# Optimization experiments

Hardware: AMD Instinct MI355X
Metric: run time of the kernel (lower is better)

## Reference

```python
import jax, jax.numpy as jnp
import numpy as np


def setup_inputs() -> dict:
    key = jax.random.key(0)
    k1, k2, k3 = jax.random.split(key, 3)
    B, V, J = 32, 100000, 52
    vertices = jax.random.normal(k1, (1, V, 3), dtype=jnp.float32)
    lbs_weights = jax.random.uniform(k2, (1, V, J), dtype=jnp.float32)
    skinning_transforms = jax.random.normal(k3, (B, J, 4, 4), dtype=jnp.float32)
    return {
        "vertices": vertices,
        "lbs_weights": lbs_weights,
        "skinning_transforms": skinning_transforms,
    }


def reference(vertices, lbs_weights, skinning_transforms):
    # 3D-vertices branch of Skinning.forward
    B = skinning_transforms.shape[0]
    J = skinning_transforms.shape[1]
    V = vertices.shape[1]
    # W: [B,V,J] (broadcast of [1,V,J]); T_flat: [B,V,16] -> T: [B,V,4,4]
    T = jnp.einsum(
        "bvj,bjx->bvx",
        jnp.broadcast_to(lbs_weights, (B, V, J)),
        skinning_transforms.reshape(B, J, 16),
    ).reshape(B, V, 4, 4)
    # homogeneous vertex coords [B,V,4]
    v_posed_homo = jnp.concatenate(
        [
            jnp.broadcast_to(vertices, (B, V, 3)),
            jnp.ones((B, V, 1), dtype=vertices.dtype),
        ],
        axis=2,
    )
    # per-vertex 4x4 @ 4 transform, keep xyz
    v_homo = jnp.einsum("bvij,bvj->bvi", T, v_posed_homo)
    return v_homo[:, :, :3]
```

## Files before the change

kernel.cpp:

```cpp
#include <hip/hip_runtime.h>
#include <hip/hip_bf16.h>


typedef __attribute__((ext_vector_type(8))) short bf16x8;
typedef __attribute__((ext_vector_type(4))) float f32x4;

constexpr int J      = 52;
constexpr int KSTEPS = 7;
constexpr int NT     = 6;
constexpr int WAVES  = 4;
constexpr int MT     = 2;
constexpr int VPW    = MT * 16;
constexpr int VPB    = WAVES * VPW;
constexpr int NSLOT  = KSTEPS * NT * 64;
constexpr int BP_B   = NSLOT * 16;
constexpr int SL_B   = 16 * VPW * 3 * 4;

__device__ __forceinline__ unsigned pk2(float a, float b) {
    __hip_bfloat162 h = __float22bfloat162_rn(make_float2(a, b));
    return *reinterpret_cast<unsigned*>(&h);
}

__global__ __launch_bounds__(256, 2) void skin_fused(
    const float* __restrict__ verts,
    const float* __restrict__ weights,
    const float* __restrict__ xf,
    float* __restrict__ out,
    int V)
{
    __shared__ __align__(16) char sBp[BP_B];
    __shared__ __align__(16) char sSl[WAVES][SL_B];

    const int tid  = threadIdx.x;
    const int lane = tid & 63;
    const int wid  = tid >> 6;
    const int lgrp = lane >> 4;
    const int lrow = lane & 15;
    const int v0   = blockIdx.x * VPB;
    const int v0w  = v0 + wid * VPW;

    float hx[MT], hy[MT], hz[MT];
    float2 wv[MT][KSTEPS];
#pragma unroll
    for (int mt = 0; mt < MT; ++mt) {
        const int v   = v0w + mt * 16 + lrow;
        const int vcl = (v < V) ? v : (V - 1);
        hx[mt] = verts[3 * (size_t)vcl + 0];
        hy[mt] = verts[3 * (size_t)vcl + 1];
        hz[mt] = verts[3 * (size_t)vcl + 2];
        const float* wr = weights + (size_t)vcl * J;
#pragma unroll
        for (int s = 0; s < KSTEPS; ++s) {
            const int j0 = s * 8 + lgrp * 2;
            wv[mt][s] = (j0 < J) ? *(const float2*)(wr + j0) : float2{0.f, 0.f};
        }
    }

    {
        const float4* __restrict__ xf4 = reinterpret_cast<const float4*>(xf);
        for (int slot = tid; slot < NSLOT; slot += 256) {
            const int s     = slot / (NT * 64);
            const int rem   = slot - s * (NT * 64);
            const int t     = rem >> 6;
            const int l     = rem & 63;
            const int plgrp = l >> 4;
            const int plrow = l & 15;
            const int n  = t * 16 + plrow;
            const int b  = n / 3;
            const int i  = n - 3 * b;
            const int j0 = s * 8 + plgrp * 2;
            float4 m0 = {0,0,0,0}, m1 = {0,0,0,0};
            if (j0 < J)     m0 = xf4[(b * J + j0) * 4 + i];
            if (j0 + 1 < J) m1 = xf4[(b * J + j0 + 1) * 4 + i];
            union { bf16x8 v; unsigned w[4]; } r;
            r.w[0] = pk2(m0.x, m0.y); r.w[1] = pk2(m0.z, m0.w);
            r.w[2] = pk2(m1.x, m1.y); r.w[3] = pk2(m1.z, m1.w);
            *(bf16x8*)(sBp + slot * 16) = r.v;
        }
    }
    __syncthreads();

    f32x4 acc[MT][NT];
#pragma unroll
    for (int mt = 0; mt < MT; ++mt)
#pragma unroll
        for (int t = 0; t < NT; ++t)
            acc[mt][t] = f32x4{0.f, 0.f, 0.f, 0.f};

#pragma unroll
    for (int s = 0; s < KSTEPS; ++s) {
        bf16x8 frag[NT];
#pragma unroll
        for (int t = 0; t < NT; ++t)
            frag[t] = *(const bf16x8*)(sBp + ((s * NT + t) * 64 + lane) * 16);
#pragma unroll
        for (int mt = 0; mt < MT; ++mt) {
            const float w0 = wv[mt][s].x, w1 = wv[mt][s].y;
            union { bf16x8 v; unsigned w[4]; } xf8;
            xf8.w[0] = pk2(w0 * hx[mt], w0 * hy[mt]);
            xf8.w[1] = pk2(w0 * hz[mt], w0);
            xf8.w[2] = pk2(w1 * hx[mt], w1 * hy[mt]);
            xf8.w[3] = pk2(w1 * hz[mt], w1);
#pragma unroll
            for (int t = 0; t < NT; ++t) {
                acc[mt][t] = __builtin_amdgcn_mfma_f32_16x16x32_bf16(
                    frag[t], xf8.v, acc[mt][t], 0, 0, 0);
            }
        }
    }

    char* const sl = sSl[wid];
    const long long validf = ((long long)V - v0w) * 3;
#pragma unroll
    for (int h = 0; h < 2; ++h) {
#pragma unroll
        for (int mt = 0; mt < MT; ++mt) {
            const int vloc = mt * 16 + lrow;
#pragma unroll
            for (int tt = 0; tt < 3; ++tt) {
                const int t = 3 * h + tt;
#pragma unroll
                for (int r = 0; r < 4; ++r) {
                    const int n  = 16 * t + lgrp * 4 + r;
                    const int b  = n / 3;
                    const int i  = n - 3 * b;
                    const int fl = ((b - 16 * h) * VPW + vloc) * 3 + i;
                    *(float*)(sl + fl * 4) = acc[mt][t][r];
                }
            }
        }
        asm volatile("s_waitcnt lgkmcnt(0)" ::: "memory");
        __builtin_amdgcn_sched_barrier(0);

        f32x4 vals[6];
#pragma unroll
        for (int q = 0; q < 6; ++q) {
            const int f = q * 64 + lane;
            vals[q] = *(const f32x4*)(sl + f * 16);
        }
        asm volatile("s_waitcnt lgkmcnt(0)" ::: "memory");
        __builtin_amdgcn_sched_barrier(0);

#pragma unroll
        for (int q = 0; q < 6; ++q) {
            const int f  = q * 64 + lane;
            const int bl = f / 24;
            const int rr = f - bl * 24;
            float* dst = out + (size_t)(16 * h + bl) * (size_t)V * 3
                             + (size_t)v0w * 3 + rr * 4;
            if ((long long)(rr + 1) * 4 <= validf) {
                *(float4*)dst = *(const float4*)&vals[q];
            } else if ((long long)rr * 4 < validf) {
#pragma unroll
                for (int e = 0; e < 4; ++e)
                    if ((long long)(rr * 4 + e) < validf) dst[e] = vals[q][e];
            }
        }
    }
}

extern "C" void kernel_launch(void* const* d_in, const int* in_sizes, int n_in,
                              void* d_out, int out_size, void* d_ws, size_t ws_size,
                              hipStream_t stream)
{
    const float* verts   = (const float*)d_in[0];
    const float* weights = (const float*)d_in[1];
    const float* xf      = (const float*)d_in[2];
    float* out = (float*)d_out;

    const int V = in_sizes[0] / 3;
    const int nblocks = (V + VPB - 1) / VPB;
    skin_fused<<<nblocks, 256, 0, stream>>>(verts, weights, xf, out, V);
}
```

Baseline: 29.26 us.

## Make skinning kernel persistent with prefetch and coalesced transform staging

Converts the one-tile-per-block kernel into a persistent grid capped at 512 blocks. Each block builds the bf16 transform fragments in LDS once and then loops over vertex tiles, prefetching the next tile's vertices and weights while it stores the current results. The transform staging now does coalesced float4 reads with scattered 8-byte LDS writes instead of strided gathers, and the output staging buffer is padded to change the LDS bank pattern. This cuts the redundant per-block transform setup, but with fewer blocks there is less latency hiding and the prefetch adds register pressure.

New measurement: 24.24 us. 1.21x faster.

```diff
diff --git a/kernel.cpp b/kernel.cpp
--- a/kernel.cpp
+++ b/kernel.cpp
@@ -6,27 +6,30 @@
 typedef __attribute__((ext_vector_type(4))) float f32x4;
 
 constexpr int J      = 52;
-constexpr int KSTEPS = 7;
 constexpr int NT     = 6;
 constexpr int WAVES  = 4;
 constexpr int MT     = 2;
 constexpr int VPW    = MT * 16;
 constexpr int VPB    = WAVES * VPW;
-constexpr int NSLOT  = KSTEPS * NT * 64;
-constexpr int BP_B   = NSLOT * 16;
-constexpr int SL_B   = 16 * VPW * 3 * 4;
+constexpr int KSTEPS = 7;
+constexpr int GMAX   = 512;
+
+constexpr int BP_B   = KSTEPS * NT * 64 * 16;
+constexpr int SPAD   = 100;
+constexpr int SL_B   = 16 * SPAD * 4;
+constexpr int NF4    = 32 * J * 4;
 
 __device__ __forceinline__ unsigned pk2(float a, float b) {
     __hip_bfloat162 h = __float22bfloat162_rn(make_float2(a, b));
     return *reinterpret_cast<unsigned*>(&h);
 }
 
-__global__ __launch_bounds__(256, 2) void skin_fused(
+__global__ __launch_bounds__(256, 2) void skin_persist(
     const float* __restrict__ verts,
     const float* __restrict__ weights,
     const float* __restrict__ xf,
     float* __restrict__ out,
-    int V)
+    int V, int ntiles, int gsize)
 {
     __shared__ __align__(16) char sBp[BP_B];
     __shared__ __align__(16) char sSl[WAVES][SL_B];
@@ -36,14 +39,14 @@
     const int wid  = tid >> 6;
     const int lgrp = lane >> 4;
     const int lrow = lane & 15;
-    const int v0   = blockIdx.x * VPB;
-    const int v0w  = v0 + wid * VPW;
+
+    int tv = blockIdx.x;
 
     float hx[MT], hy[MT], hz[MT];
     float2 wv[MT][KSTEPS];
 #pragma unroll
     for (int mt = 0; mt < MT; ++mt) {
-        const int v   = v0w + mt * 16 + lrow;
+        const int v   = tv * VPB + wid * VPW + mt * 16 + lrow;
         const int vcl = (v < V) ? v : (V - 1);
         hx[mt] = verts[3 * (size_t)vcl + 0];
         hy[mt] = verts[3 * (size_t)vcl + 1];
@@ -58,104 +61,134 @@
 
     {
         const float4* __restrict__ xf4 = reinterpret_cast<const float4*>(xf);
-        for (int slot = tid; slot < NSLOT; slot += 256) {
-            const int s     = slot / (NT * 64);
-            const int rem   = slot - s * (NT * 64);
-            const int t     = rem >> 6;
-            const int l     = rem & 63;
-            const int plgrp = l >> 4;
-            const int plrow = l & 15;
-            const int n  = t * 16 + plrow;
-            const int b  = n / 3;
-            const int i  = n - 3 * b;
-            const int j0 = s * 8 + plgrp * 2;
-            float4 m0 = {0,0,0,0}, m1 = {0,0,0,0};
-            if (j0 < J)     m0 = xf4[(b * J + j0) * 4 + i];
-            if (j0 + 1 < J) m1 = xf4[(b * J + j0 + 1) * 4 + i];
-            union { bf16x8 v; unsigned w[4]; } r;
-            r.w[0] = pk2(m0.x, m0.y); r.w[1] = pk2(m0.z, m0.w);
-            r.w[2] = pk2(m1.x, m1.y); r.w[3] = pk2(m1.z, m1.w);
-            *(bf16x8*)(sBp + slot * 16) = r.v;
+        for (int it = 0; it < NF4 / 256; ++it) {
+            const int g = it * 256 + tid;
+            const float4 m = xf4[g];
+            const int b   = g / 208;
+            const int rem = g - b * 208;
+            const int j = rem >> 2;
+            const int i = rem & 3;
+            if (i < 3) {
+                const int n    = 3 * b + i;
+                const int slot = ((j >> 3) * NT + (n >> 4)) * 64
+                               + ((j >> 1) & 3) * 16 + (n & 15);
+                uint2 d;
+                d.x = pk2(m.x, m.y);
+                d.y = pk2(m.z, m.w);
+                *(uint2*)(sBp + slot * 16 + (j & 1) * 8) = d;
+            }
+        }
+        for (int z = tid; z < NT * 32; z += 256) {
+            const int t = z >> 5, l = z & 31;
+            const int slot = (6 * NT + t) * 64 + 32 + l;
+            *(f32x4*)(sBp + slot * 16) = f32x4{0.f, 0.f, 0.f, 0.f};
         }
     }
     __syncthreads();
 
-    f32x4 acc[MT][NT];
-#pragma unroll
-    for (int mt = 0; mt < MT; ++mt)
-#pragma unroll
-        for (int t = 0; t < NT; ++t)
-            acc[mt][t] = f32x4{0.f, 0.f, 0.f, 0.f};
-
-#pragma unroll
-    for (int s = 0; s < KSTEPS; ++s) {
-        bf16x8 frag[NT];
-#pragma unroll
-        for (int t = 0; t < NT; ++t)
-            frag[t] = *(const bf16x8*)(sBp + ((s * NT + t) * 64 + lane) * 16);
-#pragma unroll
-        for (int mt = 0; mt < MT; ++mt) {
-            const float w0 = wv[mt][s].x, w1 = wv[mt][s].y;
-            union { bf16x8 v; unsigned w[4]; } xf8;
-            xf8.w[0] = pk2(w0 * hx[mt], w0 * hy[mt]);
-            xf8.w[1] = pk2(w0 * hz[mt], w0);
-            xf8.w[2] = pk2(w1 * hx[mt], w1 * hy[mt]);
-            xf8.w[3] = pk2(w1 * hz[mt], w1);
-#pragma unroll
-            for (int t = 0; t < NT; ++t) {
-                acc[mt][t] = __builtin_amdgcn_mfma_f32_16x16x32_bf16(
-                    frag[t], xf8.v, acc[mt][t], 0, 0, 0);
-            }
-        }
-    }
-
-    char* const sl = sSl[wid];
-    const long long validf = ((long long)V - v0w) * 3;
-#pragma unroll
-    for (int h = 0; h < 2; ++h) {
-#pragma unroll
-        for (int mt = 0; mt < MT; ++mt) {
-            const int vloc = mt * 16 + lrow;
-#pragma unroll
-            for (int tt = 0; tt < 3; ++tt) {
-                const int t = 3 * h + tt;
-#pragma unroll
-                for (int r = 0; r < 4; ++r) {
-                    const int n  = 16 * t + lgrp * 4 + r;
-                    const int b  = n / 3;
-                    const int i  = n - 3 * b;
-                    const int fl = ((b - 16 * h) * VPW + vloc) * 3 + i;
-                    *(float*)(sl + fl * 4) = acc[mt][t][r];
+    for (;;) {
+        f32x4 acc[MT][NT];
+#pragma unroll
+        for (int mt = 0; mt < MT; ++mt)
+#pragma unroll
+            for (int t = 0; t < NT; ++t)
+                acc[mt][t] = f32x4{0.f, 0.f, 0.f, 0.f};
+
+#pragma unroll
+        for (int s = 0; s < KSTEPS; ++s) {
+            bf16x8 frag[NT];
+#pragma unroll
+            for (int t = 0; t < NT; ++t)
+                frag[t] = *(const bf16x8*)(sBp + ((s * NT + t) * 64 + lane) * 16);
+#pragma unroll
+            for (int mt = 0; mt < MT; ++mt) {
+                const float w0 = wv[mt][s].x, w1 = wv[mt][s].y;
+                union { bf16x8 v; unsigned w[4]; } xf8;
+                xf8.w[0] = pk2(w0 * hx[mt], w0 * hy[mt]);
+                xf8.w[1] = pk2(w0 * hz[mt], w0);
+                xf8.w[2] = pk2(w1 * hx[mt], w1 * hy[mt]);
+                xf8.w[3] = pk2(w1 * hz[mt], w1);
+#pragma unroll
+                for (int t = 0; t < NT; ++t)
+                    acc[mt][t] = __builtin_amdgcn_mfma_f32_16x16x32_bf16(
+                        frag[t], xf8.v, acc[mt][t], 0, 0, 0);
+            }
+        }
+
+        const int v0w = tv * VPB + wid * VPW;
+        const long long validf = ((long long)V - v0w) * 3;
+        const int tvn = tv + gsize;
+
+        if (tvn < ntiles) {
+#pragma unroll
+            for (int mt = 0; mt < MT; ++mt) {
+                const int v   = tvn * VPB + wid * VPW + mt * 16 + lrow;
+                const int vcl = (v < V) ? v : (V - 1);
+                hx[mt] = verts[3 * (size_t)vcl + 0];
+                hy[mt] = verts[3 * (size_t)vcl + 1];
+                hz[mt] = verts[3 * (size_t)vcl + 2];
+                const float* wr = weights + (size_t)vcl * J;
+#pragma unroll
+                for (int s = 0; s < KSTEPS; ++s) {
+                    const int j0 = s * 8 + lgrp * 2;
+                    wv[mt][s] = (j0 < J) ? *(const float2*)(wr + j0)
+                                         : float2{0.f, 0.f};
                 }
             }
         }
-        asm volatile("s_waitcnt lgkmcnt(0)" ::: "memory");
-        __builtin_amdgcn_sched_barrier(0);
-
-        f32x4 vals[6];
-#pragma unroll
-        for (int q = 0; q < 6; ++q) {
-            const int f = q * 64 + lane;
-            vals[q] = *(const f32x4*)(sl + f * 16);
-        }
-        asm volatile("s_waitcnt lgkmcnt(0)" ::: "memory");
-        __builtin_amdgcn_sched_barrier(0);
-
-#pragma unroll
-        for (int q = 0; q < 6; ++q) {
-            const int f  = q * 64 + lane;
-            const int bl = f / 24;
-            const int rr = f - bl * 24;
-            float* dst = out + (size_t)(16 * h + bl) * (size_t)V * 3
-                             + (size_t)v0w * 3 + rr * 4;
-            if ((long long)(rr + 1) * 4 <= validf) {
-                *(float4*)dst = *(const float4*)&vals[q];
-            } else if ((long long)rr * 4 < validf) {
-#pragma unroll
-                for (int e = 0; e < 4; ++e)
-                    if ((long long)(rr * 4 + e) < validf) dst[e] = vals[q][e];
-            }
-        }
+
+        char* const sl = sSl[wid];
+#pragma unroll
+        for (int h = 0; h < 2; ++h) {
+#pragma unroll
+            for (int mt = 0; mt < MT; ++mt) {
+                const int vloc = mt * 16 + lrow;
+#pragma unroll
+                for (int tt = 0; tt < 3; ++tt) {
+                    const int t = 3 * h + tt;
+#pragma unroll
+                    for (int r = 0; r < 4; ++r) {
+                        const int n  = 16 * t + lgrp * 4 + r;
+                        const int b  = n / 3;
+                        const int i  = n - 3 * b;
+                        const int fl = (b - 16 * h) * SPAD + vloc * 3 + i;
+                        *(float*)(sl + fl * 4) = acc[mt][t][r];
+                    }
+                }
+            }
+            asm volatile("s_waitcnt lgkmcnt(0)" ::: "memory");
+            __builtin_amdgcn_sched_barrier(0);
+
+            f32x4 vals[6];
+#pragma unroll
+            for (int q = 0; q < 6; ++q) {
+                const int f  = q * 64 + lane;
+                const int bl = f / 24;
+                const int rr = f - bl * 24;
+                vals[q] = *(const f32x4*)(sl + bl * (SPAD * 4) + rr * 16);
+            }
+            asm volatile("s_waitcnt lgkmcnt(0)" ::: "memory");
+            __builtin_amdgcn_sched_barrier(0);
+
+#pragma unroll
+            for (int q = 0; q < 6; ++q) {
+                const int f  = q * 64 + lane;
+                const int bl = f / 24;
+                const int rr = f - bl * 24;
+                float* dst = out + (size_t)(16 * h + bl) * (size_t)V * 3
+                                 + (size_t)v0w * 3 + rr * 4;
+                if ((long long)(rr + 1) * 4 <= validf) {
+                    *(float4*)dst = *(const float4*)&vals[q];
+                } else if ((long long)rr * 4 < validf) {
+#pragma unroll
+                    for (int e = 0; e < 4; ++e)
+                        if ((long long)(rr * 4 + e) < validf) dst[e] = vals[q][e];
+                }
+            }
+        }
+
+        if (tvn >= ntiles) break;
+        tv = tvn;
     }
 }
 
@@ -169,6 +202,8 @@
     float* out = (float*)d_out;
 
     const int V = in_sizes[0] / 3;
-    const int nblocks = (V + VPB - 1) / VPB;
-    skin_fused<<<nblocks, 256, 0, stream>>>(verts, weights, xf, out, V);
+    const int ntiles = (V + VPB - 1) / VPB;
+    const int G = ntiles < GMAX ? ntiles : GMAX;
+
+    skin_persist<<<G, 256, 0, stream>>>(verts, weights, xf, out, V, ntiles, G);
 }
```

## Prepack transforms once in separate kernel and split batch halves across blocks

Applied to the files above, without the earlier changes.

Moves the per-block bf16 packing of the skinning transforms into a small pre-kernel that writes the packed fragments to workspace. The main kernel then copies only its half of the packed data straight into LDS with global_load_lds. Each vertex tile is split across two blocks, one per half of the batch, which halves accumulators, LDS and per-block stores and raises the occupancy hint to 4. The cost is an extra kernel launch and reading each vertex's weights twice, once per half.

Measured after the change: 25.34 us. 1.15x faster.

```diff
diff --git a/kernel.cpp b/kernel.cpp
--- a/kernel.cpp
+++ b/kernel.cpp
@@ -7,37 +7,80 @@
 
 constexpr int J      = 52;
 constexpr int KSTEPS = 7;
-constexpr int NT     = 6;
+constexpr int NTF    = 6;
+constexpr int NTH    = 3;
 constexpr int WAVES  = 4;
 constexpr int MT     = 2;
 constexpr int VPW    = MT * 16;
 constexpr int VPB    = WAVES * VPW;
-constexpr int NSLOT  = KSTEPS * NT * 64;
-constexpr int BP_B   = NSLOT * 16;
+constexpr int NSLOT  = KSTEPS * NTF * 64;
+constexpr int AH_CH  = KSTEPS * NTH;
 constexpr int SL_B   = 16 * VPW * 3 * 4;
+constexpr int SMEM_B = WAVES * SL_B;
+
+typedef const __attribute__((address_space(1))) char* gas1_t;
+typedef __attribute__((address_space(3))) char* las3_t;
 
 __device__ __forceinline__ unsigned pk2(float a, float b) {
     __hip_bfloat162 h = __float22bfloat162_rn(make_float2(a, b));
     return *reinterpret_cast<unsigned*>(&h);
 }
 
-__global__ __launch_bounds__(256, 2) void skin_fused(
+__global__ __launch_bounds__(256) void pack_A(
+    const float* __restrict__ xf,
+    bf16x8* __restrict__ Bp)
+{
+    const int slot = blockIdx.x * 256 + threadIdx.x;
+    if (slot >= NSLOT) return;
+    const int s    = slot / (NTF * 64);
+    const int rem  = slot - s * (NTF * 64);
+    const int t    = rem >> 6;
+    const int l    = rem & 63;
+    const int lgrp = l >> 4;
+    const int lrow = l & 15;
+    const int n = t * 16 + lrow;
+    const int b = n / 3;
+    const int i = n - 3 * b;
+    const int j0 = s * 8 + lgrp * 2;
+    const float4* __restrict__ xf4 = reinterpret_cast<const float4*>(xf);
+    float4 m0 = {0,0,0,0}, m1 = {0,0,0,0};
+    if (j0 < J)     m0 = xf4[(b * J + j0) * 4 + i];
+    if (j0 + 1 < J) m1 = xf4[(b * J + j0 + 1) * 4 + i];
+    union { bf16x8 v; unsigned w[4]; } r;
+    r.w[0] = pk2(m0.x, m0.y); r.w[1] = pk2(m0.z, m0.w);
+    r.w[2] = pk2(m1.x, m1.y); r.w[3] = pk2(m1.z, m1.w);
+    Bp[slot] = r.v;
+}
+
+__global__ __launch_bounds__(256, 4) void skin_mfma(
     const float* __restrict__ verts,
     const float* __restrict__ weights,
-    const float* __restrict__ xf,
+    const bf16x8* __restrict__ Bp,
     float* __restrict__ out,
     int V)
 {
-    __shared__ __align__(16) char sBp[BP_B];
-    __shared__ __align__(16) char sSl[WAVES][SL_B];
+    __shared__ __align__(16) char smem[SMEM_B];
 
     const int tid  = threadIdx.x;
     const int lane = tid & 63;
     const int wid  = tid >> 6;
     const int lgrp = lane >> 4;
     const int lrow = lane & 15;
-    const int v0   = blockIdx.x * VPB;
+    const int bid  = blockIdx.x;
+    const int half = bid & 1;
+    const int v0   = (bid >> 1) * VPB;
     const int v0w  = v0 + wid * VPW;
+
+    {
+        const char* g = (const char*)Bp;
+        for (int c = wid; c < AH_CH; c += WAVES) {
+            const int s  = c / NTH;
+            const int tl = c - s * NTH;
+            __builtin_amdgcn_global_load_lds(
+                (gas1_t)(g + ((s * NTF + half * NTH + tl) << 10) + lane * 16),
+                (las3_t)(smem + (c << 10)), 16, 0, 0);
+        }
+    }
 
     float hx[MT], hy[MT], hz[MT];
     float2 wv[MT][KSTEPS];
@@ -56,43 +99,21 @@
         }
     }
 
-    {
-        const float4* __restrict__ xf4 = reinterpret_cast<const float4*>(xf);
-        for (int slot = tid; slot < NSLOT; slot += 256) {
-            const int s     = slot / (NT * 64);
-            const int rem   = slot - s * (NT * 64);
-            const int t     = rem >> 6;
-            const int l     = rem & 63;
-            const int plgrp = l >> 4;
-            const int plrow = l & 15;
-            const int n  = t * 16 + plrow;
-            const int b  = n / 3;
-            const int i  = n - 3 * b;
-            const int j0 = s * 8 + plgrp * 2;
-            float4 m0 = {0,0,0,0}, m1 = {0,0,0,0};
-            if (j0 < J)     m0 = xf4[(b * J + j0) * 4 + i];
-            if (j0 + 1 < J) m1 = xf4[(b * J + j0 + 1) * 4 + i];
-            union { bf16x8 v; unsigned w[4]; } r;
-            r.w[0] = pk2(m0.x, m0.y); r.w[1] = pk2(m0.z, m0.w);
-            r.w[2] = pk2(m1.x, m1.y); r.w[3] = pk2(m1.z, m1.w);
-            *(bf16x8*)(sBp + slot * 16) = r.v;
-        }
-    }
     __syncthreads();
 
-    f32x4 acc[MT][NT];
+    f32x4 acc[MT][NTH];
 #pragma unroll
     for (int mt = 0; mt < MT; ++mt)
 #pragma unroll
-        for (int t = 0; t < NT; ++t)
+        for (int t = 0; t < NTH; ++t)
             acc[mt][t] = f32x4{0.f, 0.f, 0.f, 0.f};
 
 #pragma unroll
     for (int s = 0; s < KSTEPS; ++s) {
-        bf16x8 frag[NT];
+        bf16x8 frag[NTH];
 #pragma unroll
-        for (int t = 0; t < NT; ++t)
-            frag[t] = *(const bf16x8*)(sBp + ((s * NT + t) * 64 + lane) * 16);
+        for (int t = 0; t < NTH; ++t)
+            frag[t] = *(const bf16x8*)(smem + ((s * NTH + t) * 64 + lane) * 16);
 #pragma unroll
         for (int mt = 0; mt < MT; ++mt) {
             const float w0 = wv[mt][s].x, w1 = wv[mt][s].y;
@@ -102,59 +123,56 @@
             xf8.w[2] = pk2(w1 * hx[mt], w1 * hy[mt]);
             xf8.w[3] = pk2(w1 * hz[mt], w1);
 #pragma unroll
-            for (int t = 0; t < NT; ++t) {
+            for (int t = 0; t < NTH; ++t) {
                 acc[mt][t] = __builtin_amdgcn_mfma_f32_16x16x32_bf16(
                     frag[t], xf8.v, acc[mt][t], 0, 0, 0);
             }
         }
     }
 
-    char* const sl = sSl[wid];
+    __syncthreads();
+
+    char* const sl = smem + wid * SL_B;
     const long long validf = ((long long)V - v0w) * 3;
 #pragma unroll
-    for (int h = 0; h < 2; ++h) {
+    for (int mt = 0; mt < MT; ++mt) {
+        const int vloc = mt * 16 + lrow;
 #pragma unroll
-        for (int mt = 0; mt < MT; ++mt) {
-            const int vloc = mt * 16 + lrow;
+        for (int t = 0; t < NTH; ++t) {
 #pragma unroll
-            for (int tt = 0; tt < 3; ++tt) {
-                const int t = 3 * h + tt;
-#pragma unroll
-                for (int r = 0; r < 4; ++r) {
-                    const int n  = 16 * t + lgrp * 4 + r;
-                    const int b  = n / 3;
-                    const int i  = n - 3 * b;
-                    const int fl = ((b - 16 * h) * VPW + vloc) * 3 + i;
-                    *(float*)(sl + fl * 4) = acc[mt][t][r];
-                }
+            for (int r = 0; r < 4; ++r) {
+                const int n  = 16 * t + lgrp * 4 + r;
+                const int b  = n / 3;
+                const int i  = n - 3 * b;
+                const int fl = (b * VPW + vloc) * 3 + i;
+                *(float*)(sl + fl * 4) = acc[mt][t][r];
             }
         }
-        asm volatile("s_waitcnt lgkmcnt(0)" ::: "memory");
-        __builtin_amdgcn_sched_barrier(0);
+    }
+    asm volatile("s_waitcnt lgkmcnt(0)" ::: "memory");
+    __builtin_amdgcn_sched_barrier(0);
 
-        f32x4 vals[6];
+    f32x4 vals[6];
 #pragma unroll
-        for (int q = 0; q < 6; ++q) {
-            const int f = q * 64 + lane;
-            vals[q] = *(const f32x4*)(sl + f * 16);
-        }
-        asm volatile("s_waitcnt lgkmcnt(0)" ::: "memory");
-        __builtin_amdgcn_sched_barrier(0);
+    for (int q = 0; q < 6; ++q) {
+        const int f = q * 64 + lane;
+        vals[q] = *(const f32x4*)(sl + f * 16);
+    }
 
 #pragma unroll
-        for (int q = 0; q < 6; ++q) {
-            const int f  = q * 64 + lane;
-            const int bl = f / 24;
-            const int rr = f - bl * 24;
-            float* dst = out + (size_t)(16 * h + bl) * (size_t)V * 3
-                             + (size_t)v0w * 3 + rr * 4;
-            if ((long long)(rr + 1) * 4 <= validf) {
-                *(float4*)dst = *(const float4*)&vals[q];
-            } else if ((long long)rr * 4 < validf) {
+    for (int q = 0; q < 6; ++q) {
+        const int f  = q * 64 + lane;
+        const int bl = f / 24;
+        const int rr = f - bl * 24;
+        const int b  = half * 16 + bl;
+        float* dst = out + (size_t)b * (size_t)V * 3
+                         + (size_t)v0w * 3 + rr * 4;
+        if ((long long)(rr + 1) * 4 <= validf) {
+            *(float4*)dst = *(const float4*)&vals[q];
+        } else if ((long long)rr * 4 < validf) {
 #pragma unroll
-                for (int e = 0; e < 4; ++e)
-                    if ((long long)(rr * 4 + e) < validf) dst[e] = vals[q][e];
-            }
+            for (int e = 0; e < 4; ++e)
+                if ((long long)(rr * 4 + e) < validf) dst[e] = vals[q][e];
         }
     }
 }
@@ -169,6 +187,9 @@
     float* out = (float*)d_out;
 
     const int V = in_sizes[0] / 3;
-    const int nblocks = (V + VPB - 1) / VPB;
-    skin_fused<<<nblocks, 256, 0, stream>>>(verts, weights, xf, out, V);
+    bf16x8* Bp = (bf16x8*)d_ws;
+
+    pack_A<<<(NSLOT + 255) / 256, 256, 0, stream>>>(xf, Bp);
+    const int nvb = (V + VPB - 1) / VPB;
+    skin_mfma<<<nvb * 2, 256, 0, stream>>>(verts, weights, Bp, out, V);
 }
```
